# Kernel optimization log

Measured on AMD Instinct MI355X. Metric: run time of the kernel, lower is better.

## Reference

```python
import jax, jax.numpy as jnp
import numpy as np

HIDDEN = 896
NUM_Q_HEADS = 14
NUM_KV_HEADS = 2
HEAD_DIM = 64
ROPE_BASE = 10000.0
B, S = 4, 2048


def rotate_half(x):
    x1, x2 = jnp.split(x, 2, axis=-1)
    return jnp.concatenate((-x2, x1), axis=-1)


def rope_cos_sin(position_ids):
    # position_ids: [B, S] int -> cos/sin [B, 1, S, HEAD_DIM]
    inv_freq = 1.0 / (ROPE_BASE ** (jnp.arange(0, HEAD_DIM, 2, dtype=jnp.float32) / HEAD_DIM))
    freqs = position_ids.astype(jnp.float32)[..., None] * inv_freq  # [B,S,D/2]
    emb = jnp.concatenate((freqs, freqs), axis=-1)  # [B,S,D]
    return jnp.cos(emb)[:, None, :, :], jnp.sin(emb)[:, None, :, :]


def setup_inputs() -> dict:
    key = jax.random.key(0)
    k1, k2, k3, k4, k5 = jax.random.split(key, 5)
    s = 1.0 / np.sqrt(HIDDEN)
    return {
        "hidden_states": jax.random.normal(k1, (B, S, HIDDEN), dtype=jnp.float32),
        "position_ids": jnp.broadcast_to(jnp.arange(S, dtype=jnp.int64), (B, S)),
        "Wq": jax.random.normal(k2, (HIDDEN, NUM_Q_HEADS * HEAD_DIM), dtype=jnp.float32) * s,
        "Wk": jax.random.normal(k3, (HIDDEN, NUM_KV_HEADS * HEAD_DIM), dtype=jnp.float32) * s,
        "Wv": jax.random.normal(k4, (HIDDEN, NUM_KV_HEADS * HEAD_DIM), dtype=jnp.float32) * s,
        "Wo": jax.random.normal(k5, (NUM_Q_HEADS * HEAD_DIM, HIDDEN), dtype=jnp.float32) * s,
    }


def reference(hidden_states, position_ids, Wq, Wk, Wv, Wo):
    b, s, _ = hidden_states.shape
    n_rep = NUM_Q_HEADS // NUM_KV_HEADS

    q = (hidden_states @ Wq).reshape(b, s, NUM_Q_HEADS, HEAD_DIM).transpose(0, 2, 1, 3)   # [B,Hq,S,D]
    k = (hidden_states @ Wk).reshape(b, s, NUM_KV_HEADS, HEAD_DIM).transpose(0, 2, 1, 3)  # [B,Hkv,S,D]
    v = (hidden_states @ Wv).reshape(b, s, NUM_KV_HEADS, HEAD_DIM).transpose(0, 2, 1, 3)

    cos, sin = rope_cos_sin(position_ids)  # [B,1,S,D]
    q = q * cos + rotate_half(q) * sin
    k = k * cos + rotate_half(k) * sin

    # repeat_interleave KV heads to match query heads
    k = jnp.repeat(k, n_rep, axis=1)  # [B,Hq,S,D]
    v = jnp.repeat(v, n_rep, axis=1)

    scale = 1.0 / jnp.sqrt(jnp.float32(HEAD_DIM))
    attn = jnp.einsum('bhqd,bhkd->bhqk', q, k) * scale  # [B,Hq,S,S]
    attn = jax.nn.softmax(attn, axis=-1)
    out = jnp.einsum('bhqk,bhkd->bhqd', attn, v)  # [B,Hq,S,D]
    out = out.transpose(0, 2, 1, 3).reshape(b, s, NUM_Q_HEADS * HEAD_DIM)
    return out @ Wo
```

## Files before the change

kernel.cpp:

```cpp
#include <hip/hip_runtime.h>
#include <hip/hip_bf16.h>
#include <math.h>

typedef unsigned short ushort_t;
typedef __bf16 bf16x8 __attribute__((ext_vector_type(8)));
typedef float f32x4 __attribute__((ext_vector_type(4)));

#define HIDDEN 896
#define NQH 14
#define NKVH 2
#define HD 64
#define SEQ 2048
#define NBATCH 4

__device__ inline ushort_t f2bf(float x) {
  union { float f; unsigned u; } c; c.f = x;
  unsigned r = c.u + 0x7FFFu + ((c.u >> 16) & 1u);
  return (ushort_t)(r >> 16);
}

__device__ inline unsigned pack2bf(float a, float b) {
  union { float f; unsigned u; } ca, cb; ca.f = a; cb.f = b;
  unsigned ua = ca.u + 0x8000u, ub = cb.u + 0x8000u;
  return __builtin_amdgcn_perm(ub, ua, 0x07060302);
}

__device__ inline bf16x8 ldfrag(const ushort_t* p) {
  return *reinterpret_cast<const bf16x8*>(p);
}

__device__ inline void async16(const ushort_t* g, ushort_t* l) {
  __builtin_amdgcn_global_load_lds(
      (const __attribute__((address_space(1))) void*)g,
      (__attribute__((address_space(3))) void*)l, 16, 0, 0);
}


__device__ inline void transpose_sec(const float* __restrict__ in, ushort_t* __restrict__ out,
                                     int K, int N, int bx, int by) {
  __shared__ float tile[32][33];
  int k0 = by * 32, n0 = bx * 32;
  for (int r = threadIdx.y; r < 32; r += 8) {
    int k = k0 + r, n = n0 + threadIdx.x;
    tile[r][threadIdx.x] = (k < K && n < N) ? in[(size_t)k * N + n] : 0.f;
  }
  __syncthreads();
  for (int r = threadIdx.y; r < 32; r += 8) {
    int n = n0 + r, k = k0 + threadIdx.x;
    if (n < N && k < K) out[(size_t)n * K + k] = f2bf(tile[threadIdx.x][r]);
  }
}

__global__ void k_prep(const float* __restrict__ hidden, ushort_t* __restrict__ hb,
                       const float* __restrict__ Wq, const float* __restrict__ Wk,
                       const float* __restrict__ Wv, const float* __restrict__ Wo,
                       ushort_t* __restrict__ wT, ushort_t* __restrict__ woT,
                       float2* __restrict__ ctab) {
  const int blk = blockIdx.x;
  const int tid = threadIdx.y * 32 + threadIdx.x;
  if (blk < 7168) {
    int i = blk * 256 + tid;
    float4 v = reinterpret_cast<const float4*>(hidden)[i];
    ushort4 o;
    o.x = f2bf(v.x); o.y = f2bf(v.y); o.z = f2bf(v.z); o.w = f2bf(v.w);
    reinterpret_cast<ushort4*>(hb)[i] = o;
  } else if (blk < 7424) {
    int idx = (blk - 7168) * 256 + tid;
    int s = idx >> 5, dp = idx & 31;
    float inv = exp2f(-(float)dp * 0.41524101186092596f);
    float ang = (float)s * inv;
    float sn, cn;
    sincosf(ang, &sn, &cn);
    ctab[idx] = make_float2(cn, sn);
  } else if (blk < 8208) {
    int t = blk - 7424;
    transpose_sec(Wq, wT, 896, 896, t % 28, t / 28);
  } else if (blk < 8320) {
    int t = blk - 8208;
    transpose_sec(Wk, wT + (size_t)896 * 896, 896, 128, t % 4, t / 4);
  } else if (blk < 8432) {
    int t = blk - 8320;
    transpose_sec(Wv, wT + (size_t)1024 * 896, 896, 128, t % 4, t / 4);
  } else {
    int t = blk - 8432;
    transpose_sec(Wo, woT, 896, 896, t % 28, t / 28);
  }
}

__global__ __launch_bounds__(256) void k_qkv(
    const ushort_t* __restrict__ hb,
    const ushort_t* __restrict__ wT,
    const int* __restrict__ pos_ids,
    const float2* __restrict__ ctab,
    ushort_t* __restrict__ Qg,
    ushort_t* __restrict__ Kg,
    ushort_t* __restrict__ Vtg) {
  __shared__ ushort_t smem[8192];
  ushort_t* sa = smem;
  ushort_t* sbb = smem + 4096;

  const int f = blockIdx.x;
  const int x = f & 7, s8 = f >> 3;
  const int sect = s8 % 18;
  const int mt = (s8 / 18) * 8 + x;
  const int nt0 = sect * 64;
  const int m0 = mt * 64;
  const int tid = threadIdx.x;
  const int wave = tid >> 6, lane = tid & 63;
  const int l15 = lane & 15, quad = lane >> 4;
  const int sw = l15 & 7;

  f32x4 acc[4];
  const f32x4 z4 = {0.f, 0.f, 0.f, 0.f};
#pragma unroll
  for (int b = 0; b < 4; ++b) acc[b] = z4;

  for (int kt = 0; kt < 14; ++kt) {
    const int k0 = kt * 64;
    __syncthreads();
#pragma unroll
    for (int i = 0; i < 2; ++i) {
      int id = i * 256 + tid;
      int row = id >> 3;
      int cs = (id & 7) ^ (row & 7);
      async16(hb + (size_t)(m0 + row) * HIDDEN + k0 + cs * 8, sa + (i * 256 + wave * 64) * 8);
      async16(wT + (size_t)(nt0 + row) * HIDDEN + k0 + cs * 8, sbb + (i * 256 + wave * 64) * 8);
    }
    __syncthreads();
#pragma unroll
    for (int kc = 0; kc < 2; ++kc) {
      int c = kc * 4 + quad;
      bf16x8 af = ldfrag(sa + ((wave * 16 + l15) * 8 + (c ^ sw)) * 8);
      bf16x8 bf[4];
#pragma unroll
      for (int nb = 0; nb < 4; ++nb)
        bf[nb] = ldfrag(sbb + ((nb * 16 + l15) * 8 + (c ^ sw)) * 8);
#pragma unroll
      for (int nb = 0; nb < 4; ++nb)
        acc[nb] = __builtin_amdgcn_mfma_f32_16x16x32_bf16(af, bf[nb], acc[nb], 0, 0, 0);
    }
  }

  if (sect < 16) {
    const bool isQ = sect < 14;
    const float csc = isQ ? 0.125f * 1.4426950408889634f : 1.0f;
    ushort_t* dst = isQ ? Qg : Kg;
    const int nheads = isQ ? NQH : NKVH;
    const int hh = isQ ? sect : sect - 14;
#pragma unroll
    for (int r = 0; r < 4; ++r) {
      int token = m0 + wave * 16 + quad * 4 + r;
      int b = token >> 11, s = token & 2047;
      int pos = pos_ids[token];
      size_t base = ((size_t)(b * nheads + hh) * SEQ + s) * HD;
#pragma unroll
      for (int nb = 0; nb < 2; ++nb) {
        float2 cs = ctab[pos * 32 + nb * 16 + l15];
        float x0 = acc[nb][r];
        float x1 = acc[nb + 2][r];
        float y0 = (x0 * cs.x - x1 * cs.y) * csc;
        float y1 = (x1 * cs.x + x0 * cs.y) * csc;
        dst[base + nb * 16 + l15]      = f2bf(y0);
        dst[base + nb * 16 + l15 + 32] = f2bf(y1);
      }
    }
  } else {
    const int kvh = sect - 16;
    __syncthreads();
    ushort_t* vt = smem;
    {
      int tl = wave * 16 + quad * 4;
      int chunk = tl >> 3, ofs = tl & 7;
#pragma unroll
      for (int nb = 0; nb < 4; ++nb) {
        int row = nb * 16 + l15;
        int slot = chunk ^ (row & 7);
        ushort_t* p = vt + row * 64 + slot * 8 + ofs;
        *reinterpret_cast<unsigned*>(p)     = pack2bf(acc[nb][0], acc[nb][1]);
        *reinterpret_cast<unsigned*>(p + 2) = pack2bf(acc[nb][2], acc[nb][3]);
      }
    }
    __syncthreads();
    const int bb = m0 >> 11, s0 = m0 & 2047;
#pragma unroll
    for (int i = 0; i < 2; ++i) {
      int id = i * 256 + tid;
      int row = id >> 3, ch = id & 7;
      int slot = ch ^ (row & 7);
      uint4 v = *reinterpret_cast<const uint4*>(vt + row * 64 + slot * 8);
      *reinterpret_cast<uint4*>(Vtg + ((size_t)(bb * NKVH + kvh) * HD + row) * SEQ + s0 + ch * 8) = v;
    }
  }
}

__global__ __launch_bounds__(256) void k_attn(
    const ushort_t* __restrict__ Qg,
    const ushort_t* __restrict__ Kg,
    const ushort_t* __restrict__ Vtg,
    ushort_t* __restrict__ attn) {
  __shared__ ushort_t kbuf[2][32 * 64];
  __shared__ ushort_t vbuf[2][64 * 32];
  __shared__ ushort_t pbuf[4][32 * 40];

  const int f = blockIdx.x;
  const int x = f & 7, s8 = f >> 3;
  const int lh = s8 % 7;
  const int qt = s8 / 7;
  const int b = x >> 1, kvh = x & 1;
  const int h = kvh * 7 + lh;
  const int bh = b * NQH + h;
  const int tid = threadIdx.x;
  const int wave = tid >> 6, lane = tid & 63;
  const int l15 = lane & 15, quad = lane >> 4;
  const int q0 = qt * 128;

  bf16x8 qf[2][2];
#pragma unroll
  for (int qs = 0; qs < 2; ++qs) {
    const size_t qb = ((size_t)bh * SEQ + q0 + wave * 32 + qs * 16 + l15) * HD + quad * 8;
    qf[qs][0] = ldfrag(Qg + qb);
    qf[qs][1] = ldfrag(Qg + qb + 32);
  }

  const size_t kbase = (size_t)(b * NKVH + kvh) * SEQ * HD;
  const size_t vbase = (size_t)(b * NKVH + kvh) * HD * SEQ;

  const int krow = tid >> 3;
  const int kcs = (tid & 7) ^ (krow & 7);
  const int vrow = tid >> 2;
  const int vcs = (tid & 3) ^ (vrow & 3);
  const int sdst = wave * 512;

  float l_part[2] = {0.f, 0.f};
  f32x4 o[2][4];
  const f32x4 z4 = {0.f, 0.f, 0.f, 0.f};
#pragma unroll
  for (int qs = 0; qs < 2; ++qs)
#pragma unroll
    for (int nb = 0; nb < 4; ++nb) o[qs][nb] = z4;

  ushort_t* pw = pbuf[wave];

  auto stage = [&](int s0, ushort_t* kb, ushort_t* vb) {
    async16(Kg + kbase + (size_t)(s0 + krow) * HD + kcs * 8, kb + sdst);
    async16(Vtg + vbase + (size_t)vrow * SEQ + s0 + vcs * 8, vb + sdst);
  };

  auto compute = [&](const ushort_t* kb, const ushort_t* vb) {
#pragma unroll
    for (int nb = 0; nb < 2; ++nb) {
      int row = nb * 16 + l15;
      int swz = row & 7;
      bf16x8 kf0 = ldfrag(kb + (row * 8 + (quad ^ swz)) * 8);
      bf16x8 kf1 = ldfrag(kb + (row * 8 + ((4 + quad) ^ swz)) * 8);
#pragma unroll
      for (int qs = 0; qs < 2; ++qs) {
        f32x4 t = z4;
        t = __builtin_amdgcn_mfma_f32_16x16x32_bf16(kf0, qf[qs][0], t, 0, 0, 0);
        t = __builtin_amdgcn_mfma_f32_16x16x32_bf16(kf1, qf[qs][1], t, 0, 0, 0);
        float p0 = __builtin_amdgcn_exp2f(t[0]);
        float p1 = __builtin_amdgcn_exp2f(t[1]);
        float p2 = __builtin_amdgcn_exp2f(t[2]);
        float p3 = __builtin_amdgcn_exp2f(t[3]);
        l_part[qs] += (p0 + p1) + (p2 + p3);
        uint2 d;
        d.x = pack2bf(p0, p1);
        d.y = pack2bf(p2, p3);
        *reinterpret_cast<uint2*>(pw + (qs * 16 + l15) * 40 + nb * 16 + quad * 4) = d;
      }
    }

    bf16x8 pf[2];
#pragma unroll
    for (int qs = 0; qs < 2; ++qs)
      pf[qs] = ldfrag(pw + (qs * 16 + l15) * 40 + quad * 8);
#pragma unroll
    for (int nb = 0; nb < 4; ++nb) {
      int row = nb * 16 + l15;
      bf16x8 vf = ldfrag(vb + row * 32 + ((quad ^ (row & 3)) * 8));
#pragma unroll
      for (int qs = 0; qs < 2; ++qs)
        o[qs][nb] = __builtin_amdgcn_mfma_f32_16x16x32_bf16(pf[qs], vf, o[qs][nb], 0, 0, 0);
    }
  };

  ushort_t* k0p = kbuf[0];
  ushort_t* k1p = kbuf[1];
  ushort_t* v0p = vbuf[0];
  ushort_t* v1p = vbuf[1];

  stage(0, k0p, v0p);
  asm volatile("s_waitcnt vmcnt(0)" ::: "memory");
  __builtin_amdgcn_s_barrier();
  __builtin_amdgcn_sched_barrier(0);

  for (int jt = 0; jt < 64; ++jt) {
    int nxt = jt + 1 < 64 ? jt + 1 : 63;
    stage(nxt * 32, k1p, v1p);
    compute(k0p, v0p);
    __builtin_amdgcn_sched_barrier(0);
    asm volatile("s_waitcnt vmcnt(0)" ::: "memory");
    __builtin_amdgcn_s_barrier();
    __builtin_amdgcn_sched_barrier(0);
    ushort_t* t0 = k0p; k0p = k1p; k1p = t0;
    ushort_t* t1 = v0p; v0p = v1p; v1p = t1;
  }

#pragma unroll
  for (int qs = 0; qs < 2; ++qs) {
    float s = l_part[qs];
    s += __shfl_xor(s, 16);
    s += __shfl_xor(s, 32);
    l_part[qs] = s;
  }

#pragma unroll
  for (int qs = 0; qs < 2; ++qs) {
    float il = 1.0f / l_part[qs];
#pragma unroll
    for (int r = 0; r < 4; ++r) {
      float inv = __shfl(il, quad * 4 + r);
      int qg = q0 + wave * 32 + qs * 16 + quad * 4 + r;
#pragma unroll
      for (int nb = 0; nb < 4; ++nb) {
        float val = o[qs][nb][r] * inv;
        attn[(size_t)(b * SEQ + qg) * (NQH * HD) + h * HD + nb * 16 + l15] = f2bf(val);
      }
    }
  }
}

__global__ __launch_bounds__(256) void k_oproj(
    const ushort_t* __restrict__ attn,
    const ushort_t* __restrict__ woT,
    float* __restrict__ out) {
  __shared__ ushort_t smem[8192];
  ushort_t* sa = smem;
  ushort_t* sbb = smem + 4096;

  const int f = blockIdx.x;
  const int x = f & 7, s8 = f >> 3;
  const int n_sect = s8 % 14;
  const int mt = (s8 / 14) * 8 + x;
  const int n0 = n_sect * 64;
  const int m0 = mt * 64;
  const int tid = threadIdx.x;
  const int wave = tid >> 6, lane = tid & 63;
  const int l15 = lane & 15, quad = lane >> 4;
  const int sw = l15 & 7;

  f32x4 acc[4];
  const f32x4 z4 = {0.f, 0.f, 0.f, 0.f};
#pragma unroll
  for (int b = 0; b < 4; ++b) acc[b] = z4;

  for (int kt = 0; kt < 14; ++kt) {
    const int k0 = kt * 64;
    __syncthreads();
#pragma unroll
    for (int i = 0; i < 2; ++i) {
      int id = i * 256 + tid;
      int row = id >> 3;
      int cs = (id & 7) ^ (row & 7);
      async16(attn + (size_t)(m0 + row) * HIDDEN + k0 + cs * 8, sa + (i * 256 + wave * 64) * 8);
      async16(woT + (size_t)(n0 + row) * HIDDEN + k0 + cs * 8, sbb + (i * 256 + wave * 64) * 8);
    }
    __syncthreads();
#pragma unroll
    for (int kc = 0; kc < 2; ++kc) {
      int c = kc * 4 + quad;
      bf16x8 af = ldfrag(sa + ((wave * 16 + l15) * 8 + (c ^ sw)) * 8);
      bf16x8 bf[4];
#pragma unroll
      for (int nb = 0; nb < 4; ++nb)
        bf[nb] = ldfrag(sbb + ((nb * 16 + l15) * 8 + (c ^ sw)) * 8);
#pragma unroll
      for (int nb = 0; nb < 4; ++nb)
        acc[nb] = __builtin_amdgcn_mfma_f32_16x16x32_bf16(af, bf[nb], acc[nb], 0, 0, 0);
    }
  }

#pragma unroll
  for (int nb = 0; nb < 4; ++nb)
#pragma unroll
    for (int r = 0; r < 4; ++r)
      out[(size_t)(m0 + wave * 16 + quad * 4 + r) * HIDDEN +
          n0 + nb * 16 + l15] = acc[nb][r];
}


extern "C" void kernel_launch(void* const* d_in, const int* in_sizes, int n_in,
                              void* d_out, int out_size, void* d_ws, size_t ws_size,
                              hipStream_t stream) {
  (void)in_sizes; (void)n_in; (void)out_size; (void)ws_size;
  const float* hidden = (const float*)d_in[0];
  const int* pos      = (const int*)d_in[1];
  const float* Wq     = (const float*)d_in[2];
  const float* Wk     = (const float*)d_in[3];
  const float* Wv     = (const float*)d_in[4];
  const float* Wo     = (const float*)d_in[5];
  float* out = (float*)d_out;

  char* ws = (char*)d_ws;
  ushort_t* hb   = (ushort_t*)(ws);
  ushort_t* wT   = (ushort_t*)(ws + 14680064);
  float2*   ctab = (float2*)  (ws + 16744448);
  ushort_t* Qg   = (ushort_t*)(ws + 17268736);
  ushort_t* Kg   = (ushort_t*)(ws + 31948800);
  ushort_t* Vtg  = (ushort_t*)(ws + 34045952);
  ushort_t* attn = (ushort_t*)(ws + 36143104);
  ushort_t* woT  = (ushort_t*)(ws + 50823168);

  k_prep<<<9216, dim3(32, 8), 0, stream>>>(hidden, hb, Wq, Wk, Wv, Wo, wT, woT, ctab);
  k_qkv<<<2304, 256, 0, stream>>>(hb, wT, pos, ctab, Qg, Kg, Vtg);
  k_attn<<<896, 256, 0, stream>>>(Qg, Kg, Vtg, attn);
  k_oproj<<<1792, 256, 0, stream>>>(attn, woT, out);
}
```

Baseline: 228.5 us.

## Double M tile in QKV and output projections; change V smem swizzle

The QKV and output-projection GEMMs now compute 128-row tiles per block instead of 64. Each wave holds two 16-row A fragments and reuses the loaded B fragments across both, which halves the grid and the redundant weight-tile loads. Shared memory grows to 24KB per block and register pressure rises, while block-level parallelism drops. Separately, the attention kernel's V-tile XOR swizzle changes from row&3 to (row>>1)&3, aimed at reducing LDS bank conflicts on V fragment reads.

```diff
diff --git a/kernel.cpp b/kernel.cpp
--- a/kernel.cpp
+++ b/kernel.cpp
@@ -95,49 +95,61 @@
     ushort_t* __restrict__ Qg,
     ushort_t* __restrict__ Kg,
     ushort_t* __restrict__ Vtg) {
-  __shared__ ushort_t smem[8192];
+  __shared__ ushort_t smem[12288];
   ushort_t* sa = smem;
-  ushort_t* sbb = smem + 4096;
+  ushort_t* sbb = smem + 8192;
 
   const int f = blockIdx.x;
   const int x = f & 7, s8 = f >> 3;
   const int sect = s8 % 18;
   const int mt = (s8 / 18) * 8 + x;
   const int nt0 = sect * 64;
-  const int m0 = mt * 64;
+  const int m0 = mt * 128;
   const int tid = threadIdx.x;
   const int wave = tid >> 6, lane = tid & 63;
   const int l15 = lane & 15, quad = lane >> 4;
   const int sw = l15 & 7;
 
-  f32x4 acc[4];
+  f32x4 acc[2][4];
   const f32x4 z4 = {0.f, 0.f, 0.f, 0.f};
 #pragma unroll
-  for (int b = 0; b < 4; ++b) acc[b] = z4;
+  for (int mm = 0; mm < 2; ++mm)
+#pragma unroll
+    for (int nb = 0; nb < 4; ++nb) acc[mm][nb] = z4;
 
   for (int kt = 0; kt < 14; ++kt) {
     const int k0 = kt * 64;
     __syncthreads();
+#pragma unroll
+    for (int i = 0; i < 4; ++i) {
+      int id = i * 256 + tid;
+      int row = id >> 3;
+      int cs = (id & 7) ^ (row & 7);
+      async16(hb + (size_t)(m0 + row) * HIDDEN + k0 + cs * 8, sa + (i * 256 + wave * 64) * 8);
+    }
 #pragma unroll
     for (int i = 0; i < 2; ++i) {
       int id = i * 256 + tid;
       int row = id >> 3;
       int cs = (id & 7) ^ (row & 7);
-      async16(hb + (size_t)(m0 + row) * HIDDEN + k0 + cs * 8, sa + (i * 256 + wave * 64) * 8);
       async16(wT + (size_t)(nt0 + row) * HIDDEN + k0 + cs * 8, sbb + (i * 256 + wave * 64) * 8);
     }
     __syncthreads();
 #pragma unroll
     for (int kc = 0; kc < 2; ++kc) {
       int c = kc * 4 + quad;
-      bf16x8 af = ldfrag(sa + ((wave * 16 + l15) * 8 + (c ^ sw)) * 8);
-      bf16x8 bf[4];
+      bf16x8 af[2], bf[4];
+#pragma unroll
+      for (int mm = 0; mm < 2; ++mm)
+        af[mm] = ldfrag(sa + ((wave * 32 + mm * 16 + l15) * 8 + (c ^ sw)) * 8);
 #pragma unroll
       for (int nb = 0; nb < 4; ++nb)
         bf[nb] = ldfrag(sbb + ((nb * 16 + l15) * 8 + (c ^ sw)) * 8);
 #pragma unroll
-      for (int nb = 0; nb < 4; ++nb)
-        acc[nb] = __builtin_amdgcn_mfma_f32_16x16x32_bf16(af, bf[nb], acc[nb], 0, 0, 0);
+      for (int mm = 0; mm < 2; ++mm)
+#pragma unroll
+        for (int nb = 0; nb < 4; ++nb)
+          acc[mm][nb] = __builtin_amdgcn_mfma_f32_16x16x32_bf16(af[mm], bf[nb], acc[mm][nb], 0, 0, 0);
     }
   }
 
@@ -148,46 +160,50 @@
     const int nheads = isQ ? NQH : NKVH;
     const int hh = isQ ? sect : sect - 14;
 #pragma unroll
-    for (int r = 0; r < 4; ++r) {
-      int token = m0 + wave * 16 + quad * 4 + r;
-      int b = token >> 11, s = token & 2047;
-      int pos = pos_ids[token];
-      size_t base = ((size_t)(b * nheads + hh) * SEQ + s) * HD;
-#pragma unroll
-      for (int nb = 0; nb < 2; ++nb) {
-        float2 cs = ctab[pos * 32 + nb * 16 + l15];
-        float x0 = acc[nb][r];
-        float x1 = acc[nb + 2][r];
-        float y0 = (x0 * cs.x - x1 * cs.y) * csc;
-        float y1 = (x1 * cs.x + x0 * cs.y) * csc;
-        dst[base + nb * 16 + l15]      = f2bf(y0);
-        dst[base + nb * 16 + l15 + 32] = f2bf(y1);
+    for (int mm = 0; mm < 2; ++mm) {
+#pragma unroll
+      for (int r = 0; r < 4; ++r) {
+        int token = m0 + wave * 32 + mm * 16 + quad * 4 + r;
+        int b = token >> 11, s = token & 2047;
+        int pos = pos_ids[token];
+        size_t base = ((size_t)(b * nheads + hh) * SEQ + s) * HD;
+#pragma unroll
+        for (int nb = 0; nb < 2; ++nb) {
+          float2 cs = ctab[pos * 32 + nb * 16 + l15];
+          float x0 = acc[mm][nb][r];
+          float x1 = acc[mm][nb + 2][r];
+          float y0 = (x0 * cs.x - x1 * cs.y) * csc;
+          float y1 = (x1 * cs.x + x0 * cs.y) * csc;
+          dst[base + nb * 16 + l15]      = f2bf(y0);
+          dst[base + nb * 16 + l15 + 32] = f2bf(y1);
+        }
       }
     }
   } else {
     const int kvh = sect - 16;
     __syncthreads();
     ushort_t* vt = smem;
-    {
-      int tl = wave * 16 + quad * 4;
+#pragma unroll
+    for (int mm = 0; mm < 2; ++mm) {
+      int tl = wave * 32 + mm * 16 + quad * 4;
       int chunk = tl >> 3, ofs = tl & 7;
 #pragma unroll
       for (int nb = 0; nb < 4; ++nb) {
         int row = nb * 16 + l15;
         int slot = chunk ^ (row & 7);
-        ushort_t* p = vt + row * 64 + slot * 8 + ofs;
-        *reinterpret_cast<unsigned*>(p)     = pack2bf(acc[nb][0], acc[nb][1]);
-        *reinterpret_cast<unsigned*>(p + 2) = pack2bf(acc[nb][2], acc[nb][3]);
+        ushort_t* p = vt + row * 128 + slot * 8 + ofs;
+        *reinterpret_cast<unsigned*>(p)     = pack2bf(acc[mm][nb][0], acc[mm][nb][1]);
+        *reinterpret_cast<unsigned*>(p + 2) = pack2bf(acc[mm][nb][2], acc[mm][nb][3]);
       }
     }
     __syncthreads();
     const int bb = m0 >> 11, s0 = m0 & 2047;
 #pragma unroll
-    for (int i = 0; i < 2; ++i) {
+    for (int i = 0; i < 4; ++i) {
       int id = i * 256 + tid;
-      int row = id >> 3, ch = id & 7;
+      int row = id >> 4, ch = id & 15;
       int slot = ch ^ (row & 7);
-      uint4 v = *reinterpret_cast<const uint4*>(vt + row * 64 + slot * 8);
+      uint4 v = *reinterpret_cast<const uint4*>(vt + row * 128 + slot * 8);
       *reinterpret_cast<uint4*>(Vtg + ((size_t)(bb * NKVH + kvh) * HD + row) * SEQ + s0 + ch * 8) = v;
     }
   }
@@ -228,7 +244,7 @@
   const int krow = tid >> 3;
   const int kcs = (tid & 7) ^ (krow & 7);
   const int vrow = tid >> 2;
-  const int vcs = (tid & 3) ^ (vrow & 3);
+  const int vcs = (tid & 3) ^ ((vrow >> 1) & 3);
   const int sdst = wave * 512;
 
   float l_part[2] = {0.f, 0.f};
@@ -277,7 +293,7 @@
 #pragma unroll
     for (int nb = 0; nb < 4; ++nb) {
       int row = nb * 16 + l15;
-      bf16x8 vf = ldfrag(vb + row * 32 + ((quad ^ (row & 3)) * 8));
+      bf16x8 vf = ldfrag(vb + row * 32 + ((quad ^ ((row >> 1) & 3)) * 8));
 #pragma unroll
       for (int qs = 0; qs < 2; ++qs)
         o[qs][nb] = __builtin_amdgcn_mfma_f32_16x16x32_bf16(pf[qs], vf, o[qs][nb], 0, 0, 0);
@@ -334,58 +350,72 @@
     const ushort_t* __restrict__ attn,
     const ushort_t* __restrict__ woT,
     float* __restrict__ out) {
-  __shared__ ushort_t smem[8192];
+  __shared__ ushort_t smem[12288];
   ushort_t* sa = smem;
-  ushort_t* sbb = smem + 4096;
+  ushort_t* sbb = smem + 8192;
 
   const int f = blockIdx.x;
   const int x = f & 7, s8 = f >> 3;
   const int n_sect = s8 % 14;
   const int mt = (s8 / 14) * 8 + x;
   const int n0 = n_sect * 64;
-  const int m0 = mt * 64;
+  const int m0 = mt * 128;
   const int tid = threadIdx.x;
   const int wave = tid >> 6, lane = tid & 63;
   const int l15 = lane & 15, quad = lane >> 4;
   const int sw = l15 & 7;
 
-  f32x4 acc[4];
+  f32x4 acc[2][4];
   const f32x4 z4 = {0.f, 0.f, 0.f, 0.f};
 #pragma unroll
-  for (int b = 0; b < 4; ++b) acc[b] = z4;
+  for (int mm = 0; mm < 2; ++mm)
+#pragma unroll
+    for (int nb = 0; nb < 4; ++nb) acc[mm][nb] = z4;
 
   for (int kt = 0; kt < 14; ++kt) {
     const int k0 = kt * 64;
     __syncthreads();
+#pragma unroll
+    for (int i = 0; i < 4; ++i) {
+      int id = i * 256 + tid;
+      int row = id >> 3;
+      int cs = (id & 7) ^ (row & 7);
+      async16(attn + (size_t)(m0 + row) * HIDDEN + k0 + cs * 8, sa + (i * 256 + wave * 64) * 8);
+    }
 #pragma unroll
     for (int i = 0; i < 2; ++i) {
       int id = i * 256 + tid;
       int row = id >> 3;
       int cs = (id & 7) ^ (row & 7);
-      async16(attn + (size_t)(m0 + row) * HIDDEN + k0 + cs * 8, sa + (i * 256 + wave * 64) * 8);
       async16(woT + (size_t)(n0 + row) * HIDDEN + k0 + cs * 8, sbb + (i * 256 + wave * 64) * 8);
     }
     __syncthreads();
 #pragma unroll
     for (int kc = 0; kc < 2; ++kc) {
       int c = kc * 4 + quad;
-      bf16x8 af = ldfrag(sa + ((wave * 16 + l15) * 8 + (c ^ sw)) * 8);
-      bf16x8 bf[4];
+      bf16x8 af[2], bf[4];
+#pragma unroll
+      for (int mm = 0; mm < 2; ++mm)
+        af[mm] = ldfrag(sa + ((wave * 32 + mm * 16 + l15) * 8 + (c ^ sw)) * 8);
 #pragma unroll
       for (int nb = 0; nb < 4; ++nb)
         bf[nb] = ldfrag(sbb + ((nb * 16 + l15) * 8 + (c ^ sw)) * 8);
 #pragma unroll
-      for (int nb = 0; nb < 4; ++nb)
-        acc[nb] = __builtin_amdgcn_mfma_f32_16x16x32_bf16(af, bf[nb], acc[nb], 0, 0, 0);
-    }
-  }
-
-#pragma unroll
-  for (int nb = 0; nb < 4; ++nb)
-#pragma unroll
-    for (int r = 0; r < 4; ++r)
-      out[(size_t)(m0 + wave * 16 + quad * 4 + r) * HIDDEN +
-          n0 + nb * 16 + l15] = acc[nb][r];
+      for (int mm = 0; mm < 2; ++mm)
+#pragma unroll
+        for (int nb = 0; nb < 4; ++nb)
+          acc[mm][nb] = __builtin_amdgcn_mfma_f32_16x16x32_bf16(af[mm], bf[nb], acc[mm][nb], 0, 0, 0);
+    }
+  }
+
+#pragma unroll
+  for (int mm = 0; mm < 2; ++mm)
+#pragma unroll
+    for (int nb = 0; nb < 4; ++nb)
+#pragma unroll
+      for (int r = 0; r < 4; ++r)
+        out[(size_t)(m0 + wave * 32 + mm * 16 + quad * 4 + r) * HIDDEN +
+            n0 + nb * 16 + l15] = acc[mm][nb][r];
 }
 
 
@@ -412,7 +442,7 @@
   ushort_t* woT  = (ushort_t*)(ws + 50823168);
 
   k_prep<<<9216, dim3(32, 8), 0, stream>>>(hidden, hb, Wq, Wk, Wv, Wo, wT, woT, ctab);
-  k_qkv<<<2304, 256, 0, stream>>>(hb, wT, pos, ctab, Qg, Kg, Vtg);
+  k_qkv<<<1152, 256, 0, stream>>>(hb, wT, pos, ctab, Qg, Kg, Vtg);
   k_attn<<<896, 256, 0, stream>>>(Qg, Kg, Vtg, attn);
-  k_oproj<<<1792, 256, 0, stream>>>(attn, woT, out);
-}
+  k_oproj<<<896, 256, 0, stream>>>(attn, woT, out);
+}
```

After: 227.3 us. No clear change (-0.6%).
